# Kernel optimization log

Hardware: AMD Instinct MI355X
Metric: run time of the kernel (lower is better)

The kernel has to match this reference:

```python
import jax, jax.numpy as jnp
import numpy as np

N = 30000          # num nodes
E = 480000         # num edges (avg degree 16)
K = 3              # Chebyshev filter order
IN = 128           # input feature dim
LAMBDA_MAX = 2.0   # PyG default spectral bound
DIMS = [IN, 16, 32, 64, 128, 256, 512]


def setup_inputs() -> dict:
    key = jax.random.key(0)
    ks = jax.random.split(key, 20)
    inp = {
        "x": jax.random.normal(ks[0], (N, IN), dtype=jnp.float32),
        "edge_index": jax.random.randint(ks[1], (2, E), 0, N, dtype=jnp.int32),
        "edge_weight": jax.random.uniform(ks[2], (E,), dtype=jnp.float32),
        "batch": jnp.arange(N, dtype=jnp.int32),  # each node its own graph -> pooling is identity
    }
    for i in range(6):
        fi, fo = DIMS[i], DIMS[i + 1]
        scale = 1.0 / np.sqrt(fi * K)
        inp[f"W{i+1}"] = jax.random.normal(ks[3 + 2 * i], (K, fi, fo), dtype=jnp.float32) * scale
        inp[f"b{i+1}"] = jnp.zeros((fo,), dtype=jnp.float32)
    inp["fc_w"] = jax.random.normal(ks[16], (512, 3), dtype=jnp.float32) * 0.05
    inp["fc_b"] = jnp.zeros((3,), dtype=jnp.float32)
    return inp


def _cheb_conv(x, row, col, w_off, diag, W, b):
    """ChebConv with rw-normalized, rescaled Laplacian Lhat = 2L/lmax - I.
    Lhat @ v = scatter(w_off * v[row] -> col) + diag * v."""
    def lmv(v):
        return jax.ops.segment_sum(w_off[:, None] * v[row], col, num_segments=N) + diag * v
    Tx0 = x
    out = Tx0 @ W[0]
    Tx1 = lmv(x)
    out = out + Tx1 @ W[1]
    for k in range(2, W.shape[0]):
        Tx2 = 2.0 * lmv(Tx1) - Tx0
        out = out + Tx2 @ W[k]
        Tx0, Tx1 = Tx1, Tx2
    return out + b


def _forward(x, edge_index, edge_weight, batch, Ws, bs, fc_w, fc_b):
    row, col = edge_index[0], edge_index[1]
    # random-walk Laplacian L = I - D^{-1} A, then Lhat = 2L/lmax - I
    deg = jax.ops.segment_sum(edge_weight, row, num_segments=N)
    deg_inv = jnp.where(deg > 0, 1.0 / deg, 0.0)
    w_off = -(2.0 / LAMBDA_MAX) * deg_inv[row] * edge_weight   # off-diagonal entries of Lhat
    diag = 2.0 / LAMBDA_MAX - 1.0                               # diagonal entry of Lhat (0 for lmax=2)
    h = x
    for W, b in zip(Ws, bs):
        h = _cheb_conv(h, row, col, w_off, diag, W, b)
        h = jax.ops.segment_max(h, batch, num_segments=N)  # global_max_pool; identity since batch=arange
        h = jax.nn.softplus(h)
    return h @ fc_w + fc_b


def reference(x, edge_index, edge_weight, batch, W1, b1, W2, b2, W3, b3, W4, b4, W5, b5, W6, b6, fc_w, fc_b):
    Ws = [W1, W2, W3, W4, W5, W6]
    bs = [b1, b2, b3, b4, b5, b6]
    return _forward(x, edge_index, edge_weight, batch, Ws, bs, fc_w, fc_b)
```

## Files before the change

### kernel.cpp

```cpp
#include <hip/hip_runtime.h>
#include <math.h>
#include <stdint.h>

#define NN 30000
#define EE 480000
#define MPAD 30080
#define SCAN_B 30

typedef __attribute__((ext_vector_type(8))) short short8;
typedef __attribute__((ext_vector_type(4))) float floatx4;

__device__ __forceinline__ float b2f(ushort u) {
    union { uint u; float f; } c; c.u = ((uint)u) << 16; return c.f;
}
__device__ __forceinline__ ushort f2b(float f) {
    union { float f; uint u; } c; c.f = f;
    uint u = c.u;
    uint r = (u + 0x7FFFu + ((u >> 16) & 1u)) >> 16;
    return (ushort)r;
}
__device__ __forceinline__ float softplus_f(float x) {
    float a = fabsf(x) * 1.44269504f;
    float t = __builtin_amdgcn_exp2f(-a);
    float l = __builtin_amdgcn_logf(1.f + t);
    return fmaxf(x, 0.f) + 0.69314718f * l;
}

__device__ __forceinline__ void gld_lds16(const void* g, void* lds) {
    __builtin_amdgcn_global_load_lds(
        (__attribute__((address_space(1))) void*)(uintptr_t)(g),
        (__attribute__((address_space(3))) void*)(uint32_t)(uintptr_t)(lds),
        16, 0, 0);
}

__device__ __forceinline__ void barrier_raw() {
    __asm__ volatile("s_barrier" ::: "memory");
}
template <int N>
__device__ __forceinline__ void waitcnt_vm() {
    if constexpr (N == 0) __asm__ volatile("s_waitcnt vmcnt(0)" ::: "memory");
    else if constexpr (N == 2) __asm__ volatile("s_waitcnt vmcnt(2)" ::: "memory");
    else if constexpr (N == 3) __asm__ volatile("s_waitcnt vmcnt(3)" ::: "memory");
    else if constexpr (N == 4) __asm__ volatile("s_waitcnt vmcnt(4)" ::: "memory");
    else if constexpr (N == 8) __asm__ volatile("s_waitcnt vmcnt(8)" ::: "memory");
}

__global__ void edge_pass1(const int* __restrict__ row, const int* __restrict__ col,
                           const float* __restrict__ ew,
                           float* __restrict__ deg, int* __restrict__ counts, int E) {
    int e = blockIdx.x * blockDim.x + threadIdx.x;
    if (e >= E) return;
    atomicAdd(&deg[row[e]], ew[e]);
    atomicAdd(&counts[col[e]], 1);
}

__global__ __launch_bounds__(256) void scan_part(const int* __restrict__ counts,
                                                 int* __restrict__ bsums, int N) {
    __shared__ int s[256];
    int t = threadIdx.x;
    int base = blockIdx.x * 1024 + t * 4;
    int4 v = make_int4(0, 0, 0, 0);
    if (base + 3 < N) v = *(const int4*)(counts + base);
    else {
        if (base + 0 < N) v.x = counts[base + 0];
        if (base + 1 < N) v.y = counts[base + 1];
        if (base + 2 < N) v.z = counts[base + 2];
        if (base + 3 < N) v.w = counts[base + 3];
    }
    s[t] = v.x + v.y + v.z + v.w;
    __syncthreads();
    for (int off = 1; off < 256; off <<= 1) {
        int x = (t >= off) ? s[t - off] : 0;
        __syncthreads();
        s[t] += x;
        __syncthreads();
    }
    if (t == 255) bsums[blockIdx.x] = s[255];
}

__global__ void scan_tops(int* __restrict__ bsums) {
    int lane = threadIdx.x & 63;
    int orig = (lane < SCAN_B) ? bsums[lane] : 0;
    int v = orig;
    #pragma unroll
    for (int off = 1; off < 64; off <<= 1) {
        int x = __shfl_up(v, off);
        if (lane >= off) v += x;
    }
    if (lane < SCAN_B) bsums[lane] = v - orig;
}

__global__ __launch_bounds__(256) void scan_final(
        const int* __restrict__ counts, const int* __restrict__ bsums,
        int* __restrict__ offs, int* __restrict__ cursor, int N) {
    __shared__ int s[256];
    int t = threadIdx.x;
    int base = blockIdx.x * 1024 + t * 4;
    int4 v = make_int4(0, 0, 0, 0);
    if (base + 3 < N) v = *(const int4*)(counts + base);
    else {
        if (base + 0 < N) v.x = counts[base + 0];
        if (base + 1 < N) v.y = counts[base + 1];
        if (base + 2 < N) v.z = counts[base + 2];
        if (base + 3 < N) v.w = counts[base + 3];
    }
    int sum = v.x + v.y + v.z + v.w;
    s[t] = sum;
    __syncthreads();
    for (int off = 1; off < 256; off <<= 1) {
        int x = (t >= off) ? s[t - off] : 0;
        __syncthreads();
        s[t] += x;
        __syncthreads();
    }
    int tb = s[t] - sum + bsums[blockIdx.x];
    int4 o;
    o.x = tb;
    o.y = o.x + v.x;
    o.z = o.y + v.y;
    o.w = o.z + v.z;
    if (base + 3 < N) {
        *(int4*)(offs + base) = o;
        *(int4*)(cursor + base) = o;
    } else {
        if (base + 0 < N) { offs[base + 0] = o.x; cursor[base + 0] = o.x; }
        if (base + 1 < N) { offs[base + 1] = o.y; cursor[base + 1] = o.y; }
        if (base + 2 < N) { offs[base + 2] = o.z; cursor[base + 2] = o.z; }
        if (base + 3 < N) { offs[base + 3] = o.w; cursor[base + 3] = o.w; }
    }
    if (blockIdx.x == 0 && t == 0) offs[N] = EE;
}

__global__ void edge_pass2(const int* __restrict__ row, const int* __restrict__ col,
                           const float* __restrict__ ew, const float* __restrict__ deg,
                           int* __restrict__ cursor,
                           int* __restrict__ csr_row, float* __restrict__ csr_w, int E) {
    int e = blockIdx.x * blockDim.x + threadIdx.x;
    if (e >= E) return;
    int r = row[e];
    float d = deg[r];
    float wv = (d > 0.f) ? (-ew[e] / d) : 0.f;
    int pos = atomicAdd(&cursor[col[e]], 1);
    csr_row[pos] = r;
    csr_w[pos] = wv;
}

__global__ void copy_x_kernel(const float* __restrict__ x, ushort* __restrict__ out,
                              int total4) {
    int idx = blockIdx.x * blockDim.x + threadIdx.x;
    if (idx >= total4) return;
    float4 v = *(const float4*)(x + idx * 4);
    ushort4 o;
    o.x = f2b(v.x); o.y = f2b(v.y); o.z = f2b(v.z); o.w = f2b(v.w);
    *(ushort4*)(out + idx * 4) = o;
}

__global__ void wconv_all(const float* __restrict__ W1, const float* __restrict__ W2,
                          const float* __restrict__ W3, const float* __restrict__ W4,
                          const float* __restrict__ W5, const float* __restrict__ W6,
                          ushort* __restrict__ B1, ushort* __restrict__ B2,
                          ushort* __restrict__ B3, ushort* __restrict__ B4,
                          ushort* __restrict__ B5, ushort* __restrict__ B6) {
    int idx = blockIdx.x * blockDim.x + threadIdx.x;
    if (idx < 6144) {
        int row = idx >> 7, k = idx & 127;
        int j = row >> 4, n = row & 15;
        B1[idx] = f2b(W1[(j * 128 + k) * 16 + n]);
    } else if (idx < 8192) {
        int t = idx - 6144; int n = t >> 6, k = t & 63;
        B2[t] = f2b(k < 48 ? W2[k * 32 + n] : 0.f);
    } else if (idx < 14336) {
        int t = idx - 8192; int n = t / 96, k = t - n * 96;
        B3[t] = f2b(W3[k * 64 + n]);
    } else if (idx < 38912) {
        int t = idx - 14336; int n = t / 192, k = t - n * 192;
        B4[t] = f2b(W4[k * 128 + n]);
    } else if (idx < 137216) {
        int t = idx - 38912; int n = t / 384, k = t - n * 384;
        B5[t] = f2b(W5[k * 256 + n]);
    } else if (idx < 530432) {
        int t = idx - 137216; int n = t / 768, k = t - n * 768;
        B6[t] = f2b(W6[k * 512 + n]);
    }
}

template <int FI>
__global__ __launch_bounds__(256) void lmv_bf16(
        const ushort* __restrict__ A, ushort* __restrict__ Out,
        const ushort* __restrict__ Sub, int ldi, int ldo,
        const int* __restrict__ offs, const int* __restrict__ rows,
        const float* __restrict__ w, float scale, int N) {
    constexpr int NPW = 64 / FI;
    int wave = threadIdx.x >> 6;
    int lane = threadIdx.x & 63;
    int sub = lane / FI;
    int fbase = lane & (FI - 1);
    int node = blockIdx.x * (4 * NPW) + wave * NPW + sub;
    if (node >= N) return;
    int e0 = offs[node], e1 = offs[node + 1];
    float acc[4];
    #pragma unroll
    for (int c = 0; c < 4; ++c) acc[c] = 0.f;
    int e = e0;
    for (; e + 4 <= e1; e += 4) {
        int r0 = rows[e], r1 = rows[e + 1], r2 = rows[e + 2], r3 = rows[e + 3];
        float w0 = w[e], w1 = w[e + 1], w2 = w[e + 2], w3 = w[e + 3];
        acc[0] += w0 * b2f(A[(size_t)r0 * ldi + fbase]);
        acc[1] += w1 * b2f(A[(size_t)r1 * ldi + fbase]);
        acc[2] += w2 * b2f(A[(size_t)r2 * ldi + fbase]);
        acc[3] += w3 * b2f(A[(size_t)r3 * ldi + fbase]);
    }
    for (; e < e1; ++e)
        acc[0] += w[e] * b2f(A[(size_t)rows[e] * ldi + fbase]);
    float a = (acc[0] + acc[1]) + (acc[2] + acc[3]);
    ushort* o = Out + (size_t)node * ldo + fbase;
    if (Sub) {
        const ushort* s = Sub + (size_t)node * ldo + fbase;
        *o = f2b(scale * a - b2f(*s));
    } else {
        *o = f2b(scale * a);
    }
}

__global__ __launch_bounds__(256) void lmv_l1_final(
        const ushort* __restrict__ Z,
        const ushort* __restrict__ Y,
        const float* __restrict__ b,
        ushort* __restrict__ Out,
        const int* __restrict__ offs, const int* __restrict__ rows,
        const float* __restrict__ w, int N) {
    int wave = threadIdx.x >> 6;
    int lane = threadIdx.x & 63;
    int sub = lane >> 4, f = lane & 15;
    int node = blockIdx.x * 16 + wave * 4 + sub;
    if (node >= N) return;
    int e0 = offs[node], e1 = offs[node + 1];
    const ushort* Z2 = Z + 16;
    float acc[4];
    #pragma unroll
    for (int c = 0; c < 4; ++c) acc[c] = 0.f;
    int e = e0;
    for (; e + 4 <= e1; e += 4) {
        int r0 = rows[e], r1 = rows[e + 1], r2 = rows[e + 2], r3 = rows[e + 3];
        float w0 = w[e], w1 = w[e + 1], w2 = w[e + 2], w3 = w[e + 3];
        acc[0] += w0 * b2f(Z2[(size_t)r0 * 32 + f]);
        acc[1] += w1 * b2f(Z2[(size_t)r1 * 32 + f]);
        acc[2] += w2 * b2f(Z2[(size_t)r2 * 32 + f]);
        acc[3] += w3 * b2f(Z2[(size_t)r3 * 32 + f]);
    }
    for (; e < e1; ++e)
        acc[0] += w[e] * b2f(Z2[(size_t)rows[e] * 32 + f]);
    float z3 = (acc[0] + acc[1]) + (acc[2] + acc[3]);
    float y0 = b2f(Y[(size_t)node * 48 + f]);
    float y2 = b2f(Y[(size_t)node * 48 + 32 + f]);
    float z1 = b2f(Z[(size_t)node * 32 + f]);
    float v = y0 + z1 + 2.f * z3 - y2 + b[f];
    Out[(size_t)node * 64 + f] = f2b(softplus_f(v));
}

template <int VEC>
__global__ __launch_bounds__(256) void lmv_vec(
        const ushort* __restrict__ A, ushort* __restrict__ Out,
        const ushort* __restrict__ Sub, int ld,
        const int* __restrict__ offs, const int* __restrict__ rows,
        const float* __restrict__ w, float scale) {
    constexpr int CH = 8;
    int node = blockIdx.x * 4 + (threadIdx.x >> 6);
    int lane = threadIdx.x & 63;
    int fbase = lane * VEC;
    int e0 = __builtin_amdgcn_readfirstlane(offs[node]);
    int e1 = __builtin_amdgcn_readfirstlane(offs[node + 1]);
    float acc[CH][VEC];
    #pragma unroll
    for (int c = 0; c < CH; ++c)
        #pragma unroll
        for (int v = 0; v < VEC; ++v) acc[c][v] = 0.f;
    int e = e0;
    for (; e + CH <= e1; e += CH) {
        #pragma unroll
        for (int c = 0; c < CH; ++c) {
            int r = rows[e + c];
            float we = w[e + c];
            const ushort* pr = A + (size_t)r * ld + fbase;
            if constexpr (VEC == 4) {
                ushort4 u = *(const ushort4*)pr;
                acc[c][0] += we * b2f(u.x); acc[c][1] += we * b2f(u.y);
                acc[c][2] += we * b2f(u.z); acc[c][3] += we * b2f(u.w);
            } else if constexpr (VEC == 2) {
                ushort2 u = *(const ushort2*)pr;
                acc[c][0] += we * b2f(u.x); acc[c][1] += we * b2f(u.y);
            } else {
                acc[c][0] += we * b2f(*pr);
            }
        }
    }
    for (; e < e1; ++e) {
        int c = e & (CH - 1);
        int r = rows[e];
        float we = w[e];
        const ushort* pr = A + (size_t)r * ld + fbase;
        if constexpr (VEC == 4) {
            ushort4 u = *(const ushort4*)pr;
            acc[c][0] += we * b2f(u.x); acc[c][1] += we * b2f(u.y);
            acc[c][2] += we * b2f(u.z); acc[c][3] += we * b2f(u.w);
        } else if constexpr (VEC == 2) {
            ushort2 u = *(const ushort2*)pr;
            acc[c][0] += we * b2f(u.x); acc[c][1] += we * b2f(u.y);
        } else {
            acc[c][0] += we * b2f(*pr);
        }
    }
    #pragma unroll
    for (int c = 1; c < CH; ++c)
        #pragma unroll
        for (int v = 0; v < VEC; ++v) acc[0][v] += acc[c][v];
    ushort* o = Out + (size_t)node * ld + fbase;
    if (Sub) {
        const ushort* s = Sub + (size_t)node * ld + fbase;
        ushort tmp[VEC];
        #pragma unroll
        for (int v = 0; v < VEC; ++v) tmp[v] = f2b(scale * acc[0][v] - b2f(s[v]));
        #pragma unroll
        for (int v = 0; v < VEC; ++v) o[v] = tmp[v];
    } else {
        #pragma unroll
        for (int v = 0; v < VEC; ++v) o[v] = f2b(scale * acc[0][v]);
    }
}

template <int BN, bool ACT = true>
__global__ __launch_bounds__(256) void gemm_mfma(
        const ushort* __restrict__ A, int lda, int K,
        const ushort* __restrict__ Bt,
        const float* __restrict__ bias,
        ushort* __restrict__ Out, int ldo) {
    constexpr int BM = 128, BK = 32;
    constexpr int SM = 32;
    constexpr int FM = 2;
    constexpr int FN = BN / 16;
    constexpr int CB = BN / 16;
    constexpr int WAITN = (BN == 64) ? 3 : 2;
    __shared__ __align__(16) ushort As[2][BM][BK];
    __shared__ __align__(16) ushort Bs[2][BN][BK];
    int tid = threadIdx.x;
    int wv = tid >> 6, ln = tid & 63;
    int q = ln >> 4, r16 = ln & 15;
    int m0 = blockIdx.x * BM;

    int lrow = ln >> 2;
    int gseg = (ln & 3) ^ ((ln >> 3) & 3);
    const ushort* Abase = A + (size_t)(m0 + lrow) * lda + gseg * 8;
    const ushort* Bbase = Bt + (size_t)lrow * K + gseg * 8;

    floatx4 acc[FM][FN];
    #pragma unroll
    for (int i = 0; i < FM; ++i)
        #pragma unroll
        for (int j = 0; j < FN; ++j) acc[i][j] = (floatx4){0.f, 0.f, 0.f, 0.f};

    int sw = (q ^ ((r16 >> 1) & 3)) * 8;
    int aoff[FM], boff[FN];
    #pragma unroll
    for (int i = 0; i < FM; ++i) aoff[i] = (wv * SM + i * 16 + r16) * BK + sw;
    #pragma unroll
    for (int j = 0; j < FN; ++j) boff[j] = (j * 16 + r16) * BK + sw;

    auto stage = [&](int b, int k0) {
        gld_lds16(Abase + (size_t)(wv * 16) * lda + k0, &As[b][wv * 16][0]);
        gld_lds16(Abase + (size_t)(64 + wv * 16) * lda + k0, &As[b][64 + wv * 16][0]);
        if constexpr (CB == 4) {
            gld_lds16(Bbase + (size_t)(wv * 16) * K + k0, &Bs[b][wv * 16][0]);
        } else {
            if (wv < CB) gld_lds16(Bbase + (size_t)(wv * 16) * K + k0, &Bs[b][wv * 16][0]);
        }
    };
    auto compute = [&](int b) {
        const ushort* ldsA = &As[b][0][0];
        const ushort* ldsB = &Bs[b][0][0];
        short8 af[FM], bf[FN];
        #pragma unroll
        for (int i = 0; i < FM; ++i) af[i] = *(const short8*)(ldsA + aoff[i]);
        #pragma unroll
        for (int j = 0; j < FN; ++j) bf[j] = *(const short8*)(ldsB + boff[j]);
        #pragma unroll
        for (int i = 0; i < FM; ++i)
            #pragma unroll
            for (int j = 0; j < FN; ++j)
                acc[i][j] = __builtin_amdgcn_mfma_f32_16x16x32_bf16(
                    af[i], bf[j], acc[i][j], 0, 0, 0);
    };

    int nIter = K / BK;
    stage(0, 0);
    for (int i = 0; i < nIter; ++i) {
        int cur = i & 1;
        barrier_raw();
        if (i + 1 < nIter) {
            stage(cur ^ 1, (i + 1) * BK);
            waitcnt_vm<WAITN>();
        } else {
            waitcnt_vm<0>();
        }
        barrier_raw();
        compute(cur);
    }
    #pragma unroll
    for (int i = 0; i < FM; ++i) {
        #pragma unroll
        for (int j = 0; j < FN; ++j) {
            int n = j * 16 + r16;
            float bv = ACT ? bias[n] : 0.f;
            #pragma unroll
            for (int r = 0; r < 4; ++r) {
                int m = m0 + wv * SM + i * 16 + q * 4 + r;
                float v = acc[i][j][r] + bv;
                Out[(size_t)m * ldo + n] = f2b(ACT ? softplus_f(v) : v);
            }
        }
    }
}

template <bool FC = false, int YB = 0>
__global__ __launch_bounds__(256) void gemm_bk64(
        const ushort* __restrict__ A, int lda, int K,
        const ushort* __restrict__ Bt,
        const float* __restrict__ bias,
        ushort* __restrict__ Out, int ldo,
        const float* __restrict__ fcw, float* __restrict__ fcout) {
    constexpr int BM = 128, BN = 128, BK = 64;
    __shared__ __align__(16) ushort As[2][BM][BK];
    __shared__ __align__(16) ushort Bs[2][BN][BK];
    int tid = threadIdx.x;
    int wv = tid >> 6, ln = tid & 63;
    int wm = wv & 1, wn = wv >> 1;
    int q = ln >> 4, r16 = ln & 15;
    int nwg = gridDim.x;
    int orig = blockIdx.x;
    int xcd = orig & 7;
    int qq = nwg >> 3, rr = nwg & 7;
    int wbase = (xcd < rr) ? xcd * (qq + 1) : rr * (qq + 1) + (xcd - rr) * qq;
    int wgid = wbase + (orig >> 3);
    int yb = wgid & ((1 << YB) - 1);
    int xb = wgid >> YB;
    int m0 = xb * BM;
    int n0 = yb * BN;

    int lrow8 = ln >> 3, slds = ln & 7;
    int gseg = slds ^ lrow8;
    const ushort* Abase = A + (size_t)(m0 + lrow8) * lda + gseg * 8;
    const ushort* Bbase = Bt + (size_t)(n0 + lrow8) * K + gseg * 8;

    floatx4 acc[4][4];
    #pragma unroll
    for (int i = 0; i < 4; ++i)
        #pragma unroll
        for (int j = 0; j < 4; ++j) acc[i][j] = (floatx4){0.f, 0.f, 0.f, 0.f};

    int r7 = r16 & 7;
    int aoff[2][4], boff[2][4];
    #pragma unroll
    for (int s = 0; s < 2; ++s) {
        int segp = ((s * 4 + q) ^ r7) * 8;
        #pragma unroll
        for (int i = 0; i < 4; ++i) {
            aoff[s][i] = (wm * 64 + i * 16 + r16) * BK + segp;
            boff[s][i] = (wn * 64 + i * 16 + r16) * BK + segp;
        }
    }

    auto stage = [&](int b, int k0) {
        #pragma unroll
        for (int g = 0; g < 4; ++g)
            gld_lds16(Abase + (size_t)(wv * 8 + g * 32) * lda + k0,
                      &As[b][wv * 8 + g * 32][0]);
        #pragma unroll
        for (int g = 0; g < 4; ++g)
            gld_lds16(Bbase + (size_t)(wv * 8 + g * 32) * K + k0,
                      &Bs[b][wv * 8 + g * 32][0]);
    };
    auto compute = [&](int b) {
        const ushort* ldsA = &As[b][0][0];
        const ushort* ldsB = &Bs[b][0][0];
        #pragma unroll
        for (int s = 0; s < 2; ++s) {
            short8 af[4], bf[4];
            #pragma unroll
            for (int i = 0; i < 4; ++i) af[i] = *(const short8*)(ldsA + aoff[s][i]);
            #pragma unroll
            for (int j = 0; j < 4; ++j) bf[j] = *(const short8*)(ldsB + boff[s][j]);
            #pragma unroll
            for (int i = 0; i < 4; ++i)
                #pragma unroll
                for (int j = 0; j < 4; ++j)
                    acc[i][j] = __builtin_amdgcn_mfma_f32_16x16x32_bf16(
                        af[i], bf[j], acc[i][j], 0, 0, 0);
        }
    };

    int nIter = K / BK;
    stage(0, 0);
    for (int i = 0; i < nIter; ++i) {
        int cur = i & 1;
        barrier_raw();
        if (i + 1 < nIter) {
            stage(cur ^ 1, (i + 1) * BK);
            waitcnt_vm<8>();
        } else {
            waitcnt_vm<0>();
        }
        barrier_raw();
        compute(cur);
    }

    if constexpr (FC) {
        int pb = yb * 2 + wn;
        #pragma unroll
        for (int i = 0; i < 4; ++i) {
            #pragma unroll
            for (int r = 0; r < 4; ++r) {
                float p0 = 0.f, p1 = 0.f, p2 = 0.f;
                #pragma unroll
                for (int j = 0; j < 4; ++j) {
                    int n = n0 + wn * 64 + j * 16 + r16;
                    float v = softplus_f(acc[i][j][r] + bias[n]);
                    p0 += v * fcw[n * 3 + 0];
                    p1 += v * fcw[n * 3 + 1];
                    p2 += v * fcw[n * 3 + 2];
                }
                #pragma unroll
                for (int off = 1; off < 16; off <<= 1) {
                    p0 += __shfl_xor(p0, off);
                    p1 += __shfl_xor(p1, off);
                    p2 += __shfl_xor(p2, off);
                }
                if (r16 == 0) {
                    int m = m0 + wm * 64 + i * 16 + q * 4 + r;
                    float* dst = fcout + ((size_t)pb * MPAD + m) * 3;
                    dst[0] = p0; dst[1] = p1; dst[2] = p2;
                }
            }
        }
    } else {
        #pragma unroll
        for (int i = 0; i < 4; ++i) {
            #pragma unroll
            for (int j = 0; j < 4; ++j) {
                int n = n0 + wn * 64 + j * 16 + r16;
                float bv = bias[n];
                #pragma unroll
                for (int r = 0; r < 4; ++r) {
                    int m = m0 + wm * 64 + i * 16 + q * 4 + r;
                    Out[(size_t)m * ldo + n] = f2b(softplus_f(acc[i][j][r] + bv));
                }
            }
        }
    }
}

__global__ __launch_bounds__(256) void fc_reduce(
        const float* __restrict__ part, const float* __restrict__ fcb,
        float* __restrict__ out) {
    int idx = blockIdx.x * blockDim.x + threadIdx.x;
    if (idx >= NN * 3) return;
    int c = idx - (idx / 3) * 3;
    float s = 0.f;
    #pragma unroll
    for (int pb = 0; pb < 8; ++pb)
        s += part[(size_t)pb * MPAD * 3 + idx];
    out[idx] = s + fcb[c];
}

static inline size_t align256(size_t x) { return (x + 255) & ~(size_t)255; }

extern "C" void kernel_launch(void* const* d_in, const int* in_sizes, int n_in,
                              void* d_out, int out_size, void* d_ws, size_t ws_size,
                              hipStream_t stream) {
    const float* x   = (const float*)d_in[0];
    const int*   ei  = (const int*)d_in[1];
    const float* ew  = (const float*)d_in[2];
    const float* W[6]  = { (const float*)d_in[4],  (const float*)d_in[6],
                           (const float*)d_in[8],  (const float*)d_in[10],
                           (const float*)d_in[12], (const float*)d_in[14] };
    const float* Bv[6] = { (const float*)d_in[5],  (const float*)d_in[7],
                           (const float*)d_in[9],  (const float*)d_in[11],
                           (const float*)d_in[13], (const float*)d_in[15] };
    const float* fc_w = (const float*)d_in[16];
    const float* fc_b = (const float*)d_in[17];
    float* out = (float*)d_out;

    const int* e_row = ei;
    const int* e_col = ei + EE;

    const int fi_arr[5]   = { 16, 32, 64, 128, 256 };
    const int fo_arr[5]   = { 32, 64, 128, 256, 512 };
    const int Kpad_arr[5] = { 64, 96, 192, 384, 768 };
    const int ldo_arr[5]  = { 96, 192, 384, 768, 512 };

    char* p = (char*)d_ws;
    float* deg    = (float*)p; p += align256((size_t)NN * 4);
    int*   counts = (int*)p;   p += align256((size_t)NN * 4);
    int*   offs   = (int*)p;   p += align256((size_t)(NN + 1) * 4);
    int*   cursor = (int*)p;   p += align256((size_t)NN * 4);
    int*   bsums  = (int*)p;   p += align256((size_t)SCAN_B * 4);
    int*   csr_r  = (int*)p;   p += align256((size_t)EE * 4);
    float* csr_w  = (float*)p; p += align256((size_t)EE * 4);
    ushort* Bt1   = (ushort*)p; p += align256((size_t)48 * 128 * 2);
    ushort* Bt[5];
    for (int L = 0; L < 5; ++L) {
        Bt[L] = (ushort*)p;
        p += align256((size_t)fo_arr[L] * Kpad_arr[L] * 2);
    }
    float* fcpart = (float*)p; p += align256((size_t)8 * MPAD * 3 * 4);
    ushort* xb   = (ushort*)p; p += align256((size_t)MPAD * 128 * 2);
    ushort* Ybuf = (ushort*)p; p += align256((size_t)MPAD * 48 * 2);
    ushort* Zbuf = (ushort*)p; p += align256((size_t)MPAD * 32 * 2);
    ushort* buf0 = (ushort*)p; p += align256((size_t)MPAD * 768 * 2);
    ushort* buf1 = (ushort*)p; p += align256((size_t)MPAD * 768 * 2);
    (void)ws_size; (void)n_in; (void)in_sizes; (void)out_size;

    hipMemsetAsync(deg, 0, align256((size_t)NN * 4) + (size_t)NN * 4, stream);

    {
        int blocks = (EE + 255) / 256;
        edge_pass1<<<blocks, 256, 0, stream>>>(e_row, e_col, ew, deg, counts, EE);
        scan_part<<<SCAN_B, 256, 0, stream>>>(counts, bsums, NN);
        scan_tops<<<1, 64, 0, stream>>>(bsums);
        scan_final<<<SCAN_B, 256, 0, stream>>>(counts, bsums, offs, cursor, NN);
        edge_pass2<<<blocks, 256, 0, stream>>>(e_row, e_col, ew, deg, cursor, csr_r, csr_w, EE);
    }

    wconv_all<<<(530432 + 255) / 256, 256, 0, stream>>>(
        W[0], W[1], W[2], W[3], W[4], W[5],
        Bt1, Bt[0], Bt[1], Bt[2], Bt[3], Bt[4]);

    copy_x_kernel<<<(NN * 128 / 4 + 255) / 256, 256, 0, stream>>>(x, xb, NN * 128 / 4);

    gemm_mfma<48, false><<<dim3(MPAD / 128), 256, 0, stream>>>(
        xb, 128, 128, Bt1, nullptr, Ybuf, 48);
    lmv_bf16<32><<<(NN + 7) / 8, 256, 0, stream>>>(
        Ybuf + 16, Zbuf, nullptr, 48, 32, offs, csr_r, csr_w, 1.0f, NN);
    lmv_l1_final<<<(NN + 15) / 16, 256, 0, stream>>>(
        Zbuf, Ybuf, Bv[0], buf1, offs, csr_r, csr_w, NN);

    ushort* Abuf[5] = { buf1, buf0, buf1, buf0, buf1 };
    ushort* Obuf[5] = { buf0, buf1, buf0, buf1, buf0 };

    for (int L = 0; L < 5; ++L) {
        int fi = fi_arr[L];
        int ldA = Kpad_arr[L];
        int ldO = ldo_arr[L];
        ushort* A = Abuf[L];
        ushort* O = Obuf[L];

        switch (fi) {
            case 16:
                lmv_bf16<16><<<(NN + 15) / 16, 256, 0, stream>>>(
                    A, A + fi, nullptr, ldA, ldA, offs, csr_r, csr_w, 1.0f, NN);
                lmv_bf16<16><<<(NN + 15) / 16, 256, 0, stream>>>(
                    A + fi, A + 2 * fi, A, ldA, ldA, offs, csr_r, csr_w, 2.0f, NN);
                break;
            case 32:
                lmv_bf16<32><<<(NN + 7) / 8, 256, 0, stream>>>(
                    A, A + fi, nullptr, ldA, ldA, offs, csr_r, csr_w, 1.0f, NN);
                lmv_bf16<32><<<(NN + 7) / 8, 256, 0, stream>>>(
                    A + fi, A + 2 * fi, A, ldA, ldA, offs, csr_r, csr_w, 2.0f, NN);
                break;
            case 64:
                lmv_vec<1><<<NN / 4, 256, 0, stream>>>(
                    A, A + fi, nullptr, ldA, offs, csr_r, csr_w, 1.0f);
                lmv_vec<1><<<NN / 4, 256, 0, stream>>>(
                    A + fi, A + 2 * fi, A, ldA, offs, csr_r, csr_w, 2.0f);
                break;
            case 128:
                lmv_vec<2><<<NN / 4, 256, 0, stream>>>(
                    A, A + fi, nullptr, ldA, offs, csr_r, csr_w, 1.0f);
                lmv_vec<2><<<NN / 4, 256, 0, stream>>>(
                    A + fi, A + 2 * fi, A, ldA, offs, csr_r, csr_w, 2.0f);
                break;
            default:
                lmv_vec<4><<<NN / 4, 256, 0, stream>>>(
                    A, A + fi, nullptr, ldA, offs, csr_r, csr_w, 1.0f);
                lmv_vec<4><<<NN / 4, 256, 0, stream>>>(
                    A + fi, A + 2 * fi, A, ldA, offs, csr_r, csr_w, 2.0f);
                break;
        }

        int K = Kpad_arr[L];
        switch (fo_arr[L]) {
            case 32:
                gemm_mfma<32><<<dim3(MPAD / 128), 256, 0, stream>>>(
                    A, ldA, K, Bt[L], Bv[L + 1], O, ldO);
                break;
            case 64:
                gemm_mfma<64><<<dim3(MPAD / 128), 256, 0, stream>>>(
                    A, ldA, K, Bt[L], Bv[L + 1], O, ldO);
                break;
            case 128:
                gemm_bk64<false, 0><<<dim3(MPAD / 128), 256, 0, stream>>>(
                    A, ldA, K, Bt[L], Bv[L + 1], O, ldO, nullptr, nullptr);
                break;
            case 256:
                gemm_bk64<false, 1><<<dim3(MPAD / 128 * 2), 256, 0, stream>>>(
                    A, ldA, K, Bt[L], Bv[L + 1], O, ldO, nullptr, nullptr);
                break;
            default:
                gemm_bk64<true, 2><<<dim3(MPAD / 128 * 4), 256, 0, stream>>>(
                    A, ldA, K, Bt[L], Bv[L + 1], nullptr, 0, fc_w, fcpart);
                break;
        }
    }

    fc_reduce<<<(NN * 3 + 255) / 256, 256, 0, stream>>>(fcpart, fc_b, out);
}
```

Measured before the change: 474.6 us.

## Fuse preprocessing kernels, single-block scan, and interleave CSR row/weight pairs

Merges edge degree/count pass, x bf16 conversion and weight conversion into one heterogeneous launch, replaces the three-kernel scan with one 1024-thread block, and fuses the CSR fill with the first-layer GEMM. CSR row indices and weights are stored as interleaved int2 so each SpMV edge needs one 8-byte load instead of two. This reduces launch count and serialization in the setup phase, at the cost of a single-block scan and more complex block dispatch.

Result: faster. 463.8 us (-2.3%).

```diff
diff --git a/kernel.cpp b/kernel.cpp
--- a/kernel.cpp
+++ b/kernel.cpp
@@ -5,7 +5,6 @@
 #define NN 30000
 #define EE 480000
 #define MPAD 30080
-#define SCAN_B 30
 
 typedef __attribute__((ext_vector_type(8))) short short8;
 typedef __attribute__((ext_vector_type(4))) float floatx4;
@@ -45,294 +44,122 @@
     else if constexpr (N == 8) __asm__ volatile("s_waitcnt vmcnt(8)" ::: "memory");
 }
 
-__global__ void edge_pass1(const int* __restrict__ row, const int* __restrict__ col,
-                           const float* __restrict__ ew,
-                           float* __restrict__ deg, int* __restrict__ counts, int E) {
-    int e = blockIdx.x * blockDim.x + threadIdx.x;
-    if (e >= E) return;
-    atomicAdd(&deg[row[e]], ew[e]);
-    atomicAdd(&counts[col[e]], 1);
-}
-
-__global__ __launch_bounds__(256) void scan_part(const int* __restrict__ counts,
-                                                 int* __restrict__ bsums, int N) {
-    __shared__ int s[256];
+
+__global__ __launch_bounds__(256) void pre1_fused(
+        const int* __restrict__ row, const int* __restrict__ col,
+        const float* __restrict__ ew,
+        float* __restrict__ deg, int* __restrict__ counts,
+        const float* __restrict__ x, ushort* __restrict__ xb,
+        const float* __restrict__ W1, const float* __restrict__ W2,
+        const float* __restrict__ W3, const float* __restrict__ W4,
+        const float* __restrict__ W5, const float* __restrict__ W6,
+        ushort* __restrict__ B1, ushort* __restrict__ B2,
+        ushort* __restrict__ B3, ushort* __restrict__ B4,
+        ushort* __restrict__ B5, ushort* __restrict__ B6) {
+    int b = blockIdx.x;
+    int kind, id;
+    if (b < 7500) {
+        if ((b & 3) == 0) { kind = 0; id = b >> 2; }
+        else { kind = 1; id = (b >> 2) * 3 + (b & 3) - 1; }
+    } else { kind = 1; id = 5625 + (b - 7500); }
+    if (kind == 0) {
+        int e = id * 256 + threadIdx.x;
+        atomicAdd(&deg[row[e]], ew[e]);
+        atomicAdd(&counts[col[e]], 1);
+    } else if (id < 3750) {
+        int idx = id * 256 + threadIdx.x;
+        float4 v = *(const float4*)(x + idx * 4);
+        ushort4 o;
+        o.x = f2b(v.x); o.y = f2b(v.y); o.z = f2b(v.z); o.w = f2b(v.w);
+        *(ushort4*)(xb + idx * 4) = o;
+    } else {
+        int idx = (id - 3750) * 256 + threadIdx.x;
+        if (idx < 6144) {
+            int r = idx >> 7, k = idx & 127;
+            int j = r >> 4, n = r & 15;
+            B1[idx] = f2b(W1[(j * 128 + k) * 16 + n]);
+        } else if (idx < 8192) {
+            int t = idx - 6144; int n = t >> 6, k = t & 63;
+            B2[t] = f2b(k < 48 ? W2[k * 32 + n] : 0.f);
+        } else if (idx < 14336) {
+            int t = idx - 8192; int n = t / 96, k = t - n * 96;
+            B3[t] = f2b(W3[k * 64 + n]);
+        } else if (idx < 38912) {
+            int t = idx - 14336; int n = t / 192, k = t - n * 192;
+            B4[t] = f2b(W4[k * 128 + n]);
+        } else if (idx < 137216) {
+            int t = idx - 38912; int n = t / 384, k = t - n * 384;
+            B5[t] = f2b(W5[k * 256 + n]);
+        } else if (idx < 530432) {
+            int t = idx - 137216; int n = t / 768, k = t - n * 768;
+            B6[t] = f2b(W6[k * 512 + n]);
+        }
+    }
+}
+
+__global__ __launch_bounds__(1024) void scan_one(
+        const int* __restrict__ counts, int* __restrict__ offs,
+        int* __restrict__ cursor) {
+    __shared__ int ws[16];
     int t = threadIdx.x;
-    int base = blockIdx.x * 1024 + t * 4;
-    int4 v = make_int4(0, 0, 0, 0);
-    if (base + 3 < N) v = *(const int4*)(counts + base);
-    else {
-        if (base + 0 < N) v.x = counts[base + 0];
-        if (base + 1 < N) v.y = counts[base + 1];
-        if (base + 2 < N) v.z = counts[base + 2];
-        if (base + 3 < N) v.w = counts[base + 3];
-    }
-    s[t] = v.x + v.y + v.z + v.w;
+    int wave = t >> 6, lane = t & 63;
+    int base = t * 32;
+    int c[32];
+    int s = 0;
+    if (base < NN) {
+        #pragma unroll
+        for (int g = 0; g < 8; ++g) {
+            int4 v = *(const int4*)(counts + base + g * 4);
+            c[g * 4 + 0] = v.x; c[g * 4 + 1] = v.y;
+            c[g * 4 + 2] = v.z; c[g * 4 + 3] = v.w;
+        }
+        #pragma unroll
+        for (int i = 0; i < 32; ++i)
+            if (base + i >= NN) c[i] = 0;
+        #pragma unroll
+        for (int i = 0; i < 32; ++i) s += c[i];
+    } else {
+        #pragma unroll
+        for (int i = 0; i < 32; ++i) c[i] = 0;
+    }
+    int incl = s;
+    #pragma unroll
+    for (int off = 1; off < 64; off <<= 1) {
+        int xv = __shfl_up(incl, off);
+        if (lane >= off) incl += xv;
+    }
+    if (lane == 63) ws[wave] = incl;
     __syncthreads();
-    for (int off = 1; off < 256; off <<= 1) {
-        int x = (t >= off) ? s[t - off] : 0;
-        __syncthreads();
-        s[t] += x;
-        __syncthreads();
-    }
-    if (t == 255) bsums[blockIdx.x] = s[255];
-}
-
-__global__ void scan_tops(int* __restrict__ bsums) {
-    int lane = threadIdx.x & 63;
-    int orig = (lane < SCAN_B) ? bsums[lane] : 0;
-    int v = orig;
-    #pragma unroll
-    for (int off = 1; off < 64; off <<= 1) {
-        int x = __shfl_up(v, off);
-        if (lane >= off) v += x;
-    }
-    if (lane < SCAN_B) bsums[lane] = v - orig;
-}
-
-__global__ __launch_bounds__(256) void scan_final(
-        const int* __restrict__ counts, const int* __restrict__ bsums,
-        int* __restrict__ offs, int* __restrict__ cursor, int N) {
-    __shared__ int s[256];
-    int t = threadIdx.x;
-    int base = blockIdx.x * 1024 + t * 4;
-    int4 v = make_int4(0, 0, 0, 0);
-    if (base + 3 < N) v = *(const int4*)(counts + base);
-    else {
-        if (base + 0 < N) v.x = counts[base + 0];
-        if (base + 1 < N) v.y = counts[base + 1];
-        if (base + 2 < N) v.z = counts[base + 2];
-        if (base + 3 < N) v.w = counts[base + 3];
-    }
-    int sum = v.x + v.y + v.z + v.w;
-    s[t] = sum;
+    if (wave == 0) {
+        int v = (lane < 16) ? ws[lane] : 0;
+        #pragma unroll
+        for (int off = 1; off < 16; off <<= 1) {
+            int xv = __shfl_up(v, off);
+            if (lane >= off) v += xv;
+        }
+        if (lane < 16) ws[lane] = v;
+    }
     __syncthreads();
-    for (int off = 1; off < 256; off <<= 1) {
-        int x = (t >= off) ? s[t - off] : 0;
-        __syncthreads();
-        s[t] += x;
-        __syncthreads();
-    }
-    int tb = s[t] - sum + bsums[blockIdx.x];
-    int4 o;
-    o.x = tb;
-    o.y = o.x + v.x;
-    o.z = o.y + v.y;
-    o.w = o.z + v.z;
-    if (base + 3 < N) {
-        *(int4*)(offs + base) = o;
-        *(int4*)(cursor + base) = o;
-    } else {
-        if (base + 0 < N) { offs[base + 0] = o.x; cursor[base + 0] = o.x; }
-        if (base + 1 < N) { offs[base + 1] = o.y; cursor[base + 1] = o.y; }
-        if (base + 2 < N) { offs[base + 2] = o.z; cursor[base + 2] = o.z; }
-        if (base + 3 < N) { offs[base + 3] = o.w; cursor[base + 3] = o.w; }
-    }
-    if (blockIdx.x == 0 && t == 0) offs[N] = EE;
-}
-
-__global__ void edge_pass2(const int* __restrict__ row, const int* __restrict__ col,
-                           const float* __restrict__ ew, const float* __restrict__ deg,
-                           int* __restrict__ cursor,
-                           int* __restrict__ csr_row, float* __restrict__ csr_w, int E) {
-    int e = blockIdx.x * blockDim.x + threadIdx.x;
-    if (e >= E) return;
-    int r = row[e];
-    float d = deg[r];
-    float wv = (d > 0.f) ? (-ew[e] / d) : 0.f;
-    int pos = atomicAdd(&cursor[col[e]], 1);
-    csr_row[pos] = r;
-    csr_w[pos] = wv;
-}
-
-__global__ void copy_x_kernel(const float* __restrict__ x, ushort* __restrict__ out,
-                              int total4) {
-    int idx = blockIdx.x * blockDim.x + threadIdx.x;
-    if (idx >= total4) return;
-    float4 v = *(const float4*)(x + idx * 4);
-    ushort4 o;
-    o.x = f2b(v.x); o.y = f2b(v.y); o.z = f2b(v.z); o.w = f2b(v.w);
-    *(ushort4*)(out + idx * 4) = o;
-}
-
-__global__ void wconv_all(const float* __restrict__ W1, const float* __restrict__ W2,
-                          const float* __restrict__ W3, const float* __restrict__ W4,
-                          const float* __restrict__ W5, const float* __restrict__ W6,
-                          ushort* __restrict__ B1, ushort* __restrict__ B2,
-                          ushort* __restrict__ B3, ushort* __restrict__ B4,
-                          ushort* __restrict__ B5, ushort* __restrict__ B6) {
-    int idx = blockIdx.x * blockDim.x + threadIdx.x;
-    if (idx < 6144) {
-        int row = idx >> 7, k = idx & 127;
-        int j = row >> 4, n = row & 15;
-        B1[idx] = f2b(W1[(j * 128 + k) * 16 + n]);
-    } else if (idx < 8192) {
-        int t = idx - 6144; int n = t >> 6, k = t & 63;
-        B2[t] = f2b(k < 48 ? W2[k * 32 + n] : 0.f);
-    } else if (idx < 14336) {
-        int t = idx - 8192; int n = t / 96, k = t - n * 96;
-        B3[t] = f2b(W3[k * 64 + n]);
-    } else if (idx < 38912) {
-        int t = idx - 14336; int n = t / 192, k = t - n * 192;
-        B4[t] = f2b(W4[k * 128 + n]);
-    } else if (idx < 137216) {
-        int t = idx - 38912; int n = t / 384, k = t - n * 384;
-        B5[t] = f2b(W5[k * 256 + n]);
-    } else if (idx < 530432) {
-        int t = idx - 137216; int n = t / 768, k = t - n * 768;
-        B6[t] = f2b(W6[k * 512 + n]);
-    }
-}
-
-template <int FI>
-__global__ __launch_bounds__(256) void lmv_bf16(
-        const ushort* __restrict__ A, ushort* __restrict__ Out,
-        const ushort* __restrict__ Sub, int ldi, int ldo,
-        const int* __restrict__ offs, const int* __restrict__ rows,
-        const float* __restrict__ w, float scale, int N) {
-    constexpr int NPW = 64 / FI;
-    int wave = threadIdx.x >> 6;
-    int lane = threadIdx.x & 63;
-    int sub = lane / FI;
-    int fbase = lane & (FI - 1);
-    int node = blockIdx.x * (4 * NPW) + wave * NPW + sub;
-    if (node >= N) return;
-    int e0 = offs[node], e1 = offs[node + 1];
-    float acc[4];
-    #pragma unroll
-    for (int c = 0; c < 4; ++c) acc[c] = 0.f;
-    int e = e0;
-    for (; e + 4 <= e1; e += 4) {
-        int r0 = rows[e], r1 = rows[e + 1], r2 = rows[e + 2], r3 = rows[e + 3];
-        float w0 = w[e], w1 = w[e + 1], w2 = w[e + 2], w3 = w[e + 3];
-        acc[0] += w0 * b2f(A[(size_t)r0 * ldi + fbase]);
-        acc[1] += w1 * b2f(A[(size_t)r1 * ldi + fbase]);
-        acc[2] += w2 * b2f(A[(size_t)r2 * ldi + fbase]);
-        acc[3] += w3 * b2f(A[(size_t)r3 * ldi + fbase]);
-    }
-    for (; e < e1; ++e)
-        acc[0] += w[e] * b2f(A[(size_t)rows[e] * ldi + fbase]);
-    float a = (acc[0] + acc[1]) + (acc[2] + acc[3]);
-    ushort* o = Out + (size_t)node * ldo + fbase;
-    if (Sub) {
-        const ushort* s = Sub + (size_t)node * ldo + fbase;
-        *o = f2b(scale * a - b2f(*s));
-    } else {
-        *o = f2b(scale * a);
-    }
-}
-
-__global__ __launch_bounds__(256) void lmv_l1_final(
-        const ushort* __restrict__ Z,
-        const ushort* __restrict__ Y,
-        const float* __restrict__ b,
-        ushort* __restrict__ Out,
-        const int* __restrict__ offs, const int* __restrict__ rows,
-        const float* __restrict__ w, int N) {
-    int wave = threadIdx.x >> 6;
-    int lane = threadIdx.x & 63;
-    int sub = lane >> 4, f = lane & 15;
-    int node = blockIdx.x * 16 + wave * 4 + sub;
-    if (node >= N) return;
-    int e0 = offs[node], e1 = offs[node + 1];
-    const ushort* Z2 = Z + 16;
-    float acc[4];
-    #pragma unroll
-    for (int c = 0; c < 4; ++c) acc[c] = 0.f;
-    int e = e0;
-    for (; e + 4 <= e1; e += 4) {
-        int r0 = rows[e], r1 = rows[e + 1], r2 = rows[e + 2], r3 = rows[e + 3];
-        float w0 = w[e], w1 = w[e + 1], w2 = w[e + 2], w3 = w[e + 3];
-        acc[0] += w0 * b2f(Z2[(size_t)r0 * 32 + f]);
-        acc[1] += w1 * b2f(Z2[(size_t)r1 * 32 + f]);
-        acc[2] += w2 * b2f(Z2[(size_t)r2 * 32 + f]);
-        acc[3] += w3 * b2f(Z2[(size_t)r3 * 32 + f]);
-    }
-    for (; e < e1; ++e)
-        acc[0] += w[e] * b2f(Z2[(size_t)rows[e] * 32 + f]);
-    float z3 = (acc[0] + acc[1]) + (acc[2] + acc[3]);
-    float y0 = b2f(Y[(size_t)node * 48 + f]);
-    float y2 = b2f(Y[(size_t)node * 48 + 32 + f]);
-    float z1 = b2f(Z[(size_t)node * 32 + f]);
-    float v = y0 + z1 + 2.f * z3 - y2 + b[f];
-    Out[(size_t)node * 64 + f] = f2b(softplus_f(v));
-}
-
-template <int VEC>
-__global__ __launch_bounds__(256) void lmv_vec(
-        const ushort* __restrict__ A, ushort* __restrict__ Out,
-        const ushort* __restrict__ Sub, int ld,
-        const int* __restrict__ offs, const int* __restrict__ rows,
-        const float* __restrict__ w, float scale) {
-    constexpr int CH = 8;
-    int node = blockIdx.x * 4 + (threadIdx.x >> 6);
-    int lane = threadIdx.x & 63;
-    int fbase = lane * VEC;
-    int e0 = __builtin_amdgcn_readfirstlane(offs[node]);
-    int e1 = __builtin_amdgcn_readfirstlane(offs[node + 1]);
-    float acc[CH][VEC];
-    #pragma unroll
-    for (int c = 0; c < CH; ++c)
-        #pragma unroll
-        for (int v = 0; v < VEC; ++v) acc[c][v] = 0.f;
-    int e = e0;
-    for (; e + CH <= e1; e += CH) {
-        #pragma unroll
-        for (int c = 0; c < CH; ++c) {
-            int r = rows[e + c];
-            float we = w[e + c];
-            const ushort* pr = A + (size_t)r * ld + fbase;
-            if constexpr (VEC == 4) {
-                ushort4 u = *(const ushort4*)pr;
-                acc[c][0] += we * b2f(u.x); acc[c][1] += we * b2f(u.y);
-                acc[c][2] += we * b2f(u.z); acc[c][3] += we * b2f(u.w);
-            } else if constexpr (VEC == 2) {
-                ushort2 u = *(const ushort2*)pr;
-                acc[c][0] += we * b2f(u.x); acc[c][1] += we * b2f(u.y);
-            } else {
-                acc[c][0] += we * b2f(*pr);
-            }
-        }
-    }
-    for (; e < e1; ++e) {
-        int c = e & (CH - 1);
-        int r = rows[e];
-        float we = w[e];
-        const ushort* pr = A + (size_t)r * ld + fbase;
-        if constexpr (VEC == 4) {
-            ushort4 u = *(const ushort4*)pr;
-            acc[c][0] += we * b2f(u.x); acc[c][1] += we * b2f(u.y);
-            acc[c][2] += we * b2f(u.z); acc[c][3] += we * b2f(u.w);
-        } else if constexpr (VEC == 2) {
-            ushort2 u = *(const ushort2*)pr;
-            acc[c][0] += we * b2f(u.x); acc[c][1] += we * b2f(u.y);
-        } else {
-            acc[c][0] += we * b2f(*pr);
-        }
-    }
-    #pragma unroll
-    for (int c = 1; c < CH; ++c)
-        #pragma unroll
-        for (int v = 0; v < VEC; ++v) acc[0][v] += acc[c][v];
-    ushort* o = Out + (size_t)node * ld + fbase;
-    if (Sub) {
-        const ushort* s = Sub + (size_t)node * ld + fbase;
-        ushort tmp[VEC];
-        #pragma unroll
-        for (int v = 0; v < VEC; ++v) tmp[v] = f2b(scale * acc[0][v] - b2f(s[v]));
-        #pragma unroll
-        for (int v = 0; v < VEC; ++v) o[v] = tmp[v];
-    } else {
-        #pragma unroll
-        for (int v = 0; v < VEC; ++v) o[v] = f2b(scale * acc[0][v]);
-    }
-}
-
-template <int BN, bool ACT = true>
-__global__ __launch_bounds__(256) void gemm_mfma(
-        const ushort* __restrict__ A, int lda, int K,
-        const ushort* __restrict__ Bt,
-        const float* __restrict__ bias,
+    int wbase = (wave == 0) ? 0 : ws[wave - 1];
+    int run = wbase + incl - s;
+    if (base < NN) {
+        int o[32];
+        #pragma unroll
+        for (int i = 0; i < 32; ++i) { o[i] = run; run += c[i]; }
+        #pragma unroll
+        for (int g = 0; g < 8; ++g) {
+            int4 v = make_int4(o[g * 4], o[g * 4 + 1], o[g * 4 + 2], o[g * 4 + 3]);
+            *(int4*)(offs + base + g * 4) = v;
+            *(int4*)(cursor + base + g * 4) = v;
+        }
+    }
+    if (t == 0) offs[NN] = EE;
+}
+
+template <int BN, bool ACT>
+__device__ __forceinline__ void gemm_mfma_body(
+        int bid, const ushort* __restrict__ A, int lda, int K,
+        const ushort* __restrict__ Bt, const float* __restrict__ bias,
         ushort* __restrict__ Out, int ldo) {
     constexpr int BM = 128, BK = 32;
     constexpr int SM = 32;
@@ -345,7 +172,7 @@
     int tid = threadIdx.x;
     int wv = tid >> 6, ln = tid & 63;
     int q = ln >> 4, r16 = ln & 15;
-    int m0 = blockIdx.x * BM;
+    int m0 = bid * BM;
 
     int lrow = ln >> 2;
     int gseg = (ln & 3) ^ ((ln >> 3) & 3);
@@ -417,6 +244,181 @@
                 Out[(size_t)m * ldo + n] = f2b(ACT ? softplus_f(v) : v);
             }
         }
+    }
+}
+
+template <int BN, bool ACT = true>
+__global__ __launch_bounds__(256) void gemm_mfma(
+        const ushort* __restrict__ A, int lda, int K,
+        const ushort* __restrict__ Bt,
+        const float* __restrict__ bias,
+        ushort* __restrict__ Out, int ldo) {
+    gemm_mfma_body<BN, ACT>(blockIdx.x, A, lda, K, Bt, bias, Out, ldo);
+}
+
+__global__ __launch_bounds__(256) void pre2_fused(
+        const int* __restrict__ row, const int* __restrict__ col,
+        const float* __restrict__ ew, const float* __restrict__ deg,
+        int* __restrict__ cursor, int2* __restrict__ csr_rw,
+        const ushort* __restrict__ xb, const ushort* __restrict__ Bt1,
+        ushort* __restrict__ Ybuf) {
+    int b = blockIdx.x;
+    if (b < MPAD / 128) {
+        gemm_mfma_body<48, false>(b, xb, 128, 128, Bt1, nullptr, Ybuf, 48);
+    } else {
+        int e = (b - MPAD / 128) * 256 + threadIdx.x;
+        int r = row[e];
+        float d = deg[r];
+        float wv = (d > 0.f) ? (-ew[e] / d) : 0.f;
+        int pos = atomicAdd(&cursor[col[e]], 1);
+        csr_rw[pos] = make_int2(r, __float_as_int(wv));
+    }
+}
+
+template <int FI>
+__global__ __launch_bounds__(256) void lmv_bf16(
+        const ushort* __restrict__ A, ushort* __restrict__ Out,
+        const ushort* __restrict__ Sub, int ldi, int ldo,
+        const int* __restrict__ offs, const int2* __restrict__ rw,
+        float scale, int N) {
+    constexpr int NPW = 64 / FI;
+    int wave = threadIdx.x >> 6;
+    int lane = threadIdx.x & 63;
+    int sub = lane / FI;
+    int fbase = lane & (FI - 1);
+    int node = blockIdx.x * (4 * NPW) + wave * NPW + sub;
+    if (node >= N) return;
+    int e0 = offs[node], e1 = offs[node + 1];
+    float acc[4];
+    #pragma unroll
+    for (int c = 0; c < 4; ++c) acc[c] = 0.f;
+    int e = e0;
+    for (; e + 4 <= e1; e += 4) {
+        int2 u0 = rw[e], u1 = rw[e + 1], u2 = rw[e + 2], u3 = rw[e + 3];
+        acc[0] += __int_as_float(u0.y) * b2f(A[(size_t)u0.x * ldi + fbase]);
+        acc[1] += __int_as_float(u1.y) * b2f(A[(size_t)u1.x * ldi + fbase]);
+        acc[2] += __int_as_float(u2.y) * b2f(A[(size_t)u2.x * ldi + fbase]);
+        acc[3] += __int_as_float(u3.y) * b2f(A[(size_t)u3.x * ldi + fbase]);
+    }
+    for (; e < e1; ++e) {
+        int2 u = rw[e];
+        acc[0] += __int_as_float(u.y) * b2f(A[(size_t)u.x * ldi + fbase]);
+    }
+    float a = (acc[0] + acc[1]) + (acc[2] + acc[3]);
+    ushort* o = Out + (size_t)node * ldo + fbase;
+    if (Sub) {
+        const ushort* s = Sub + (size_t)node * ldo + fbase;
+        *o = f2b(scale * a - b2f(*s));
+    } else {
+        *o = f2b(scale * a);
+    }
+}
+
+__global__ __launch_bounds__(256) void lmv_l1_final(
+        const ushort* __restrict__ Z,
+        const ushort* __restrict__ Y,
+        const float* __restrict__ b,
+        ushort* __restrict__ Out,
+        const int* __restrict__ offs, const int2* __restrict__ rw, int N) {
+    int wave = threadIdx.x >> 6;
+    int lane = threadIdx.x & 63;
+    int sub = lane >> 4, f = lane & 15;
+    int node = blockIdx.x * 16 + wave * 4 + sub;
+    if (node >= N) return;
+    int e0 = offs[node], e1 = offs[node + 1];
+    const ushort* Z2 = Z + 16;
+    float acc[4];
+    #pragma unroll
+    for (int c = 0; c < 4; ++c) acc[c] = 0.f;
+    int e = e0;
+    for (; e + 4 <= e1; e += 4) {
+        int2 u0 = rw[e], u1 = rw[e + 1], u2 = rw[e + 2], u3 = rw[e + 3];
+        acc[0] += __int_as_float(u0.y) * b2f(Z2[(size_t)u0.x * 32 + f]);
+        acc[1] += __int_as_float(u1.y) * b2f(Z2[(size_t)u1.x * 32 + f]);
+        acc[2] += __int_as_float(u2.y) * b2f(Z2[(size_t)u2.x * 32 + f]);
+        acc[3] += __int_as_float(u3.y) * b2f(Z2[(size_t)u3.x * 32 + f]);
+    }
+    for (; e < e1; ++e) {
+        int2 u = rw[e];
+        acc[0] += __int_as_float(u.y) * b2f(Z2[(size_t)u.x * 32 + f]);
+    }
+    float z3 = (acc[0] + acc[1]) + (acc[2] + acc[3]);
+    float y0 = b2f(Y[(size_t)node * 48 + f]);
+    float y2 = b2f(Y[(size_t)node * 48 + 32 + f]);
+    float z1 = b2f(Z[(size_t)node * 32 + f]);
+    float v = y0 + z1 + 2.f * z3 - y2 + b[f];
+    Out[(size_t)node * 64 + f] = f2b(softplus_f(v));
+}
+
+template <int VEC>
+__global__ __launch_bounds__(256) void lmv_vec(
+        const ushort* __restrict__ A, ushort* __restrict__ Out,
+        const ushort* __restrict__ Sub, int ld,
+        const int* __restrict__ offs, const int2* __restrict__ rw,
+        float scale) {
+    constexpr int CH = 8;
+    int node = blockIdx.x * 4 + (threadIdx.x >> 6);
+    int lane = threadIdx.x & 63;
+    int fbase = lane * VEC;
+    int e0 = __builtin_amdgcn_readfirstlane(offs[node]);
+    int e1 = __builtin_amdgcn_readfirstlane(offs[node + 1]);
+    float acc[CH][VEC];
+    #pragma unroll
+    for (int c = 0; c < CH; ++c)
+        #pragma unroll
+        for (int v = 0; v < VEC; ++v) acc[c][v] = 0.f;
+    int e = e0;
+    for (; e + CH <= e1; e += CH) {
+        #pragma unroll
+        for (int c = 0; c < CH; ++c) {
+            int2 u = rw[e + c];
+            int r = u.x;
+            float we = __int_as_float(u.y);
+            const ushort* pr = A + (size_t)r * ld + fbase;
+            if constexpr (VEC == 4) {
+                ushort4 uu = *(const ushort4*)pr;
+                acc[c][0] += we * b2f(uu.x); acc[c][1] += we * b2f(uu.y);
+                acc[c][2] += we * b2f(uu.z); acc[c][3] += we * b2f(uu.w);
+            } else if constexpr (VEC == 2) {
+                ushort2 uu = *(const ushort2*)pr;
+                acc[c][0] += we * b2f(uu.x); acc[c][1] += we * b2f(uu.y);
+            } else {
+                acc[c][0] += we * b2f(*pr);
+            }
+        }
+    }
+    for (; e < e1; ++e) {
+        int c = e & (CH - 1);
+        int2 u = rw[e];
+        int r = u.x;
+        float we = __int_as_float(u.y);
+        const ushort* pr = A + (size_t)r * ld + fbase;
+        if constexpr (VEC == 4) {
+            ushort4 uu = *(const ushort4*)pr;
+            acc[c][0] += we * b2f(uu.x); acc[c][1] += we * b2f(uu.y);
+            acc[c][2] += we * b2f(uu.z); acc[c][3] += we * b2f(uu.w);
+        } else if constexpr (VEC == 2) {
+            ushort2 uu = *(const ushort2*)pr;
+            acc[c][0] += we * b2f(uu.x); acc[c][1] += we * b2f(uu.y);
+        } else {
+            acc[c][0] += we * b2f(*pr);
+        }
+    }
+    #pragma unroll
+    for (int c = 1; c < CH; ++c)
+        #pragma unroll
+        for (int v = 0; v < VEC; ++v) acc[0][v] += acc[c][v];
+    ushort* o = Out + (size_t)node * ld + fbase;
+    if (Sub) {
+        const ushort* s = Sub + (size_t)node * ld + fbase;
+        ushort tmp[VEC];
+        #pragma unroll
+        for (int v = 0; v < VEC; ++v) tmp[v] = f2b(scale * acc[0][v] - b2f(s[v]));
+        #pragma unroll
+        for (int v = 0; v < VEC; ++v) o[v] = tmp[v];
+    } else {
+        #pragma unroll
+        for (int v = 0; v < VEC; ++v) o[v] = f2b(scale * acc[0][v]);
     }
 }
 
@@ -601,9 +603,7 @@
     int*   counts = (int*)p;   p += align256((size_t)NN * 4);
     int*   offs   = (int*)p;   p += align256((size_t)(NN + 1) * 4);
     int*   cursor = (int*)p;   p += align256((size_t)NN * 4);
-    int*   bsums  = (int*)p;   p += align256((size_t)SCAN_B * 4);
-    int*   csr_r  = (int*)p;   p += align256((size_t)EE * 4);
-    float* csr_w  = (float*)p; p += align256((size_t)EE * 4);
+    int2*  csr_rw = (int2*)p;  p += align256((size_t)EE * 8);
     ushort* Bt1   = (ushort*)p; p += align256((size_t)48 * 128 * 2);
     ushort* Bt[5];
     for (int L = 0; L < 5; ++L) {
@@ -620,27 +620,20 @@
 
     hipMemsetAsync(deg, 0, align256((size_t)NN * 4) + (size_t)NN * 4, stream);
 
-    {
-        int blocks = (EE + 255) / 256;
-        edge_pass1<<<blocks, 256, 0, stream>>>(e_row, e_col, ew, deg, counts, EE);
-        scan_part<<<SCAN_B, 256, 0, stream>>>(counts, bsums, NN);
-        scan_tops<<<1, 64, 0, stream>>>(bsums);
-        scan_final<<<SCAN_B, 256, 0, stream>>>(counts, bsums, offs, cursor, NN);
-        edge_pass2<<<blocks, 256, 0, stream>>>(e_row, e_col, ew, deg, cursor, csr_r, csr_w, EE);
-    }
-
-    wconv_all<<<(530432 + 255) / 256, 256, 0, stream>>>(
+    pre1_fused<<<7697, 256, 0, stream>>>(
+        e_row, e_col, ew, deg, counts, x, xb,
         W[0], W[1], W[2], W[3], W[4], W[5],
         Bt1, Bt[0], Bt[1], Bt[2], Bt[3], Bt[4]);
 
-    copy_x_kernel<<<(NN * 128 / 4 + 255) / 256, 256, 0, stream>>>(x, xb, NN * 128 / 4);
-
-    gemm_mfma<48, false><<<dim3(MPAD / 128), 256, 0, stream>>>(
-        xb, 128, 128, Bt1, nullptr, Ybuf, 48);
+    scan_one<<<1, 1024, 0, stream>>>(counts, offs, cursor);
+
+    pre2_fused<<<MPAD / 128 + EE / 256, 256, 0, stream>>>(
+        e_row, e_col, ew, deg, cursor, csr_rw, xb, Bt1, Ybuf);
+
     lmv_bf16<32><<<(NN + 7) / 8, 256, 0, stream>>>(
-        Ybuf + 16, Zbuf, nullptr, 48, 32, offs, csr_r, csr_w, 1.0f, NN);
+        Ybuf + 16, Zbuf, nullptr, 48, 32, offs, csr_rw, 1.0f, NN);
     lmv_l1_final<<<(NN + 15) / 16, 256, 0, stream>>>(
-        Zbuf, Ybuf, Bv[0], buf1, offs, csr_r, csr_w, NN);
+        Zbuf, Ybuf, Bv[0], buf1, offs, csr_rw, NN);
 
     ushort* Abuf[5] = { buf1, buf0, buf1, buf0, buf1 };
     ushort* Obuf[5] = { buf0, buf1, buf0, buf1, buf0 };
@@ -655,33 +648,33 @@
         switch (fi) {
             case 16:
                 lmv_bf16<16><<<(NN + 15) / 16, 256, 0, stream>>>(
-                    A, A + fi, nullptr, ldA, ldA, offs, csr_r, csr_w, 1.0f, NN);
+                    A, A + fi, nullptr, ldA, ldA, offs, csr_rw, 1.0f, NN);
                 lmv_bf16<16><<<(NN + 15) / 16, 256, 0, stream>>>(
-                    A + fi, A + 2 * fi, A, ldA, ldA, offs, csr_r, csr_w, 2.0f, NN);
+                    A + fi, A + 2 * fi, A, ldA, ldA, offs, csr_rw, 2.0f, NN);
                 break;
             case 32:
                 lmv_bf16<32><<<(NN + 7) / 8, 256, 0, stream>>>(
-                    A, A + fi, nullptr, ldA, ldA, offs, csr_r, csr_w, 1.0f, NN);
+                    A, A + fi, nullptr, ldA, ldA, offs, csr_rw, 1.0f, NN);
                 lmv_bf16<32><<<(NN + 7) / 8, 256, 0, stream>>>(
-                    A + fi, A + 2 * fi, A, ldA, ldA, offs, csr_r, csr_w, 2.0f, NN);
+                    A + fi, A + 2 * fi, A, ldA, ldA, offs, csr_rw, 2.0f, NN);
                 break;
             case 64:
                 lmv_vec<1><<<NN / 4, 256, 0, stream>>>(
-                    A, A + fi, nullptr, ldA, offs, csr_r, csr_w, 1.0f);
+                    A, A + fi, nullptr, ldA, offs, csr_rw, 1.0f);
                 lmv_vec<1><<<NN / 4, 256, 0, stream>>>(
-                    A + fi, A + 2 * fi, A, ldA, offs, csr_r, csr_w, 2.0f);
+                    A + fi, A + 2 * fi, A, ldA, offs, csr_rw, 2.0f);
                 break;
             case 128:
                 lmv_vec<2><<<NN / 4, 256, 0, stream>>>(
-                    A, A + fi, nullptr, ldA, offs, csr_r, csr_w, 1.0f);
+                    A, A + fi, nullptr, ldA, offs, csr_rw, 1.0f);
                 lmv_vec<2><<<NN / 4, 256, 0, stream>>>(
-                    A + fi, A + 2 * fi, A, ldA, offs, csr_r, csr_w, 2.0f);
+                    A + fi, A + 2 * fi, A, ldA, offs, csr_rw, 2.0f);
                 break;
             default:
                 lmv_vec<4><<<NN / 4, 256, 0, stream>>>(
-                    A, A + fi, nullptr, ldA, offs, csr_r, csr_w, 1.0f);
+                    A, A + fi, nullptr, ldA, offs, csr_rw, 1.0f);
                 lmv_vec<4><<<NN / 4, 256, 0, stream>>>(
-                    A + fi, A + 2 * fi, A, ldA, offs, csr_r, csr_w, 2.0f);
+                    A + fi, A + 2 * fi, A, ldA, offs, csr_rw, 2.0f);
                 break;
         }
 
```
